# Kernel tuning notes

Measured on AMD Instinct MI355X. Metric: run time of the kernel, lower is better.

Reference implementation:

```python
import jax, jax.numpy as jnp
import numpy as np

jax.config.update("jax_enable_x64", True)  # needed for faithful float64 bit reinterpretation

VOCAB = 50257
HIDDEN = 1024
MAX_POS = 4096
TYPE_VOCAB = 2
NUM_FEATS = 94
PROJ_INTER = 256
NUM_TOKEN_ID = 5
LN_EPS = 1e-12


def _layer_norm(x, g, b, eps=LN_EPS):
    mu = jnp.mean(x, axis=-1, keepdims=True)
    var = jnp.var(x, axis=-1, keepdims=True)
    return (x - mu) * jax.lax.rsqrt(var + eps) * g + b


def _numeric_features(values, formats):
    # values: [B,S] float32 (torch casts to float64 internally), formats: [B,S] int
    v = values.astype(jnp.float64)
    # float64_binary_repr (64 bits). Torch: (int64_view & (1<<i)) > 0; bit 63 mask
    # overflows to INT64_MIN so (x & mask) > 0 is always False -> replicate exactly.
    bits = jax.lax.bitcast_convert_type(v, jnp.int64)
    masks = jnp.left_shift(jnp.int64(1), jnp.arange(64, dtype=jnp.int64))
    binary = ((bits[..., None] & masks) > 0).astype(jnp.float32)  # [B,S,64]
    av = jnp.abs(v)
    fl = jnp.floor(av)
    units = jnp.clip(fl % 10.0, 0, 9).astype(jnp.int32)
    oh_units = jax.nn.one_hot(units, 10, dtype=jnp.float32)       # [B,S,10]
    tens = jnp.clip((fl // 10.0) % 10.0, 0, 9).astype(jnp.int32)
    oh_tens = jax.nn.one_hot(tens, 10, dtype=jnp.float32)         # [B,S,10]
    log_v = jnp.log(av + 1e-6).astype(jnp.float32)
    sign = jnp.sign(v).astype(jnp.float32)
    expo = jnp.where(av > 1e-6, jnp.floor(jnp.log10(jnp.maximum(av, 1e-300))), 0.0).astype(jnp.float32)
    is_int = (av == fl).astype(jnp.float32)
    is_pos = (v > 0).astype(jnp.float32)
    is_zero = (v == 0.0).astype(jnp.float32)
    is_neg = (v < 0).astype(jnp.float32)
    pos_int = (v == jnp.floor(v)) & (v > 0)
    l2 = jnp.log2(jnp.maximum(v, 1.0))
    is_pow2 = (pos_int & (l2 == jnp.floor(l2))).astype(jnp.float32)
    fmt_int = (formats == 0).astype(jnp.float32)
    fmt_float = (formats == 1).astype(jnp.float32)
    scalars = jnp.stack([log_v, sign, expo, is_int, is_pos, is_zero, is_neg, is_pow2, fmt_int, fmt_float], axis=-1)
    return jnp.concatenate([binary, oh_units, oh_tens, scalars], axis=-1)  # [B,S,94]


def setup_inputs() -> dict:
    key = jax.random.key(0)
    ks = jax.random.split(key, 12)
    B, S = 8, 2048
    input_ids = jax.random.randint(ks[0], (B, S), 0, VOCAB, dtype=jnp.int64)
    numeric_values = jax.random.normal(ks[1], (B, S), dtype=jnp.float32) * 100.0
    numeric_formats = jax.random.randint(ks[2], (B, S), 0, 2, dtype=jnp.int64)
    s = 0.02
    W_word = (jax.random.normal(ks[3], (VOCAB, HIDDEN), dtype=jnp.float32) * s).at[0].set(0.0)  # padding_idx=0
    W_pos = jax.random.normal(ks[4], (MAX_POS, HIDDEN), dtype=jnp.float32) * s
    W_type = jax.random.normal(ks[5], (TYPE_VOCAB, HIDDEN), dtype=jnp.float32) * s
    ln_g = jnp.ones((HIDDEN,), jnp.float32)
    ln_b = jnp.zeros((HIDDEN,), jnp.float32)
    p_w1 = jax.random.normal(ks[6], (NUM_FEATS, PROJ_INTER), dtype=jnp.float32) * s
    p_b1 = jnp.zeros((PROJ_INTER,), jnp.float32)
    p_w2 = jax.random.normal(ks[7], (PROJ_INTER, HIDDEN), dtype=jnp.float32) * s
    p_b2 = jnp.zeros((HIDDEN,), jnp.float32)
    pln_g = jnp.ones((HIDDEN,), jnp.float32)
    pln_b = jnp.zeros((HIDDEN,), jnp.float32)
    return dict(input_ids=input_ids, numeric_values=numeric_values, numeric_formats=numeric_formats,
                W_word=W_word, W_pos=W_pos, W_type=W_type, ln_g=ln_g, ln_b=ln_b,
                p_w1=p_w1, p_b1=p_b1, p_w2=p_w2, p_b2=p_b2, pln_g=pln_g, pln_b=pln_b)


def reference(input_ids, numeric_values, numeric_formats, W_word, W_pos, W_type,
              ln_g, ln_b, p_w1, p_b1, p_w2, p_b2, pln_g, pln_b):
    B, S = input_ids.shape
    # text embeddings: word + position + token_type (token_type_ids default = 0)
    text = W_word[input_ids] + W_pos[jnp.arange(S)][None, :, :] + W_type[0][None, None, :]
    text = text.astype(jnp.float32)
    # active numeric positions: [NUM] token AND non-NaN value
    active = (input_ids == NUM_TOKEN_ID) & ~jnp.isnan(numeric_values)  # [B,S]
    safe_vals = jnp.where(active, numeric_values, 1.0)
    feats = _numeric_features(safe_vals, numeric_formats)  # [B,S,94] float32
    # numeric projection MLP: Linear -> GELU -> Linear -> LayerNorm
    h = jax.nn.gelu(feats @ p_w1 + p_b1, approximate=False)
    num_emb = _layer_norm(h @ p_w2 + p_b2, pln_g, pln_b)
    num_emb = jnp.where(active[..., None], num_emb, 0.0)  # scatter into zeros
    # fusion_type == 'add', then final LayerNorm (dropout p=0 -> identity)
    out = _layer_norm(text + num_emb, ln_g, ln_b)
    return out
```

## Files before the change

kernel.cpp:

```cpp
#include <hip/hip_runtime.h>
#include <math.h>

#define HIDDEN 1024
#define SEQ 2048
#define NF 94
#define PI 256
#define NUM_TOKEN 5

typedef float vfloat4 __attribute__((ext_vector_type(4)));

__device__ __forceinline__ float gelu_exact(float a) {
    return 0.5f * a * (1.0f + erff(a * 0.70710678118654752f));
}

__global__ __launch_bounds__(256)
void blackhole_emb_kernel(const int* __restrict__ ids,
                          const float* __restrict__ vals,
                          const int* __restrict__ fmts,
                          const float* __restrict__ Ww,
                          const float* __restrict__ Wp,
                          const float* __restrict__ Wt,
                          const float* __restrict__ lng,
                          const float* __restrict__ lnb,
                          const float* __restrict__ w1,
                          const float* __restrict__ b1,
                          const float* __restrict__ w2,
                          const float* __restrict__ b2,
                          const float* __restrict__ plng,
                          const float* __restrict__ plnb,
                          float* __restrict__ out,
                          int tokens)
{
    const int lane  = threadIdx.x & 63;
    const int wv    = threadIdx.x >> 6;
    const int token = blockIdx.x * 4 + wv;
    if (token >= tokens) return;
    const int s = token & (SEQ - 1);

    const int   id     = ids[token];
    const float vraw   = vals[token];
    const bool  active = (id == NUM_TOKEN) && !isnan(vraw);

    const float* wrow = Ww + (size_t)id * HIDDEN;
    const float* prow = Wp + (size_t)s  * HIDDEN;
    const int    col0 = lane * 4;

    float x[4][4];
    #pragma unroll
    for (int j = 0; j < 4; ++j) {
        const int off = j * 256 + col0;
        const float4 aw = *(const float4*)(wrow + off);
        const float4 ap = *(const float4*)(prow + off);
        const float4 at = *(const float4*)(Wt   + off);
        x[j][0] = aw.x + ap.x + at.x;
        x[j][1] = aw.y + ap.y + at.y;
        x[j][2] = aw.z + ap.z + at.z;
        x[j][3] = aw.w + ap.w + at.w;
    }

    if (active) {
        const double    v    = (double)vraw;
        const double    av   = fabs(v);
        const long long bits = __double_as_longlong(v);
        const double    fl   = floor(av);
        const int       fmt  = fmts[token];

        float f0 = (lane < 63 && ((bits >> lane) & 1LL)) ? 1.0f : 0.0f;
        float f1 = 0.0f;
        if (lane < 10) {
            const int units = (int)fmin(fmax(fmod(fl, 10.0), 0.0), 9.0);
            f1 = (lane == units) ? 1.0f : 0.0f;
        } else if (lane < 20) {
            const int tens = (int)fmin(fmax(fmod(floor(fl / 10.0), 10.0), 0.0), 9.0);
            f1 = (lane - 10 == tens) ? 1.0f : 0.0f;
        } else if (lane < 30) {
            switch (lane - 20) {
                case 0: f1 = (float)log(av + 1e-6); break;
                case 1: f1 = (v > 0.0) ? 1.0f : ((v < 0.0) ? -1.0f : 0.0f); break;
                case 2: f1 = (av > 1e-6) ? (float)floor(log10(fmax(av, 1e-300))) : 0.0f; break;
                case 3: f1 = (av == fl) ? 1.0f : 0.0f; break;
                case 4: f1 = (v > 0.0) ? 1.0f : 0.0f; break;
                case 5: f1 = (v == 0.0) ? 1.0f : 0.0f; break;
                case 6: f1 = (v < 0.0) ? 1.0f : 0.0f; break;
                case 7: {
                    const bool   pos_int = (v == floor(v)) && (v > 0.0);
                    const double l2      = log2(fmax(v, 1.0));
                    f1 = (pos_int && (l2 == floor(l2))) ? 1.0f : 0.0f;
                    break;
                }
                case 8: f1 = (fmt == 0) ? 1.0f : 0.0f; break;
                case 9: f1 = (fmt == 1) ? 1.0f : 0.0f; break;
            }
        }

        float acc[4] = { b1[lane], b1[lane + 64], b1[lane + 128], b1[lane + 192] };
        for (int k = 0; k < 64; ++k) {
            const float  fk  = __shfl(f0, k, 64);
            const float* col = w1 + k * PI;
            acc[0] = fmaf(fk, col[lane],       acc[0]);
            acc[1] = fmaf(fk, col[lane + 64],  acc[1]);
            acc[2] = fmaf(fk, col[lane + 128], acc[2]);
            acc[3] = fmaf(fk, col[lane + 192], acc[3]);
        }
        for (int k = 0; k < NF - 64; ++k) {
            const float  fk  = __shfl(f1, k, 64);
            const float* col = w1 + (64 + k) * PI;
            acc[0] = fmaf(fk, col[lane],       acc[0]);
            acc[1] = fmaf(fk, col[lane + 64],  acc[1]);
            acc[2] = fmaf(fk, col[lane + 128], acc[2]);
            acc[3] = fmaf(fk, col[lane + 192], acc[3]);
        }
        float h[4];
        #pragma unroll
        for (int i = 0; i < 4; ++i) h[i] = gelu_exact(acc[i]);

        float n[4][4];
        #pragma unroll
        for (int j = 0; j < 4; ++j) {
            const float4 bb = *(const float4*)(b2 + j * 256 + col0);
            n[j][0] = bb.x; n[j][1] = bb.y; n[j][2] = bb.z; n[j][3] = bb.w;
        }
        #pragma unroll
        for (int i = 0; i < 4; ++i) {
            for (int kk = 0; kk < 64; ++kk) {
                const float  hk  = __shfl(h[i], kk, 64);
                const float* row = w2 + (size_t)(i * 64 + kk) * HIDDEN;
                #pragma unroll
                for (int j = 0; j < 4; ++j) {
                    const float4 w = *(const float4*)(row + j * 256 + col0);
                    n[j][0] = fmaf(hk, w.x, n[j][0]);
                    n[j][1] = fmaf(hk, w.y, n[j][1]);
                    n[j][2] = fmaf(hk, w.z, n[j][2]);
                    n[j][3] = fmaf(hk, w.w, n[j][3]);
                }
            }
        }

        float sm = 0.0f, sq = 0.0f;
        #pragma unroll
        for (int j = 0; j < 4; ++j)
            #pragma unroll
            for (int c = 0; c < 4; ++c) { sm += n[j][c]; sq += n[j][c] * n[j][c]; }
        #pragma unroll
        for (int off = 32; off > 0; off >>= 1) {
            sm += __shfl_xor(sm, off, 64);
            sq += __shfl_xor(sq, off, 64);
        }
        const float mu   = sm * (1.0f / HIDDEN);
        const float var  = sq * (1.0f / HIDDEN) - mu * mu;
        const float rstd = rsqrtf(var + 1e-12f);
        #pragma unroll
        for (int j = 0; j < 4; ++j) {
            const float4 g4 = *(const float4*)(plng + j * 256 + col0);
            const float4 b4 = *(const float4*)(plnb + j * 256 + col0);
            x[j][0] += (n[j][0] - mu) * rstd * g4.x + b4.x;
            x[j][1] += (n[j][1] - mu) * rstd * g4.y + b4.y;
            x[j][2] += (n[j][2] - mu) * rstd * g4.z + b4.z;
            x[j][3] += (n[j][3] - mu) * rstd * g4.w + b4.w;
        }
    }

    float sm = 0.0f, sq = 0.0f;
    #pragma unroll
    for (int j = 0; j < 4; ++j)
        #pragma unroll
        for (int c = 0; c < 4; ++c) { sm += x[j][c]; sq += x[j][c] * x[j][c]; }
    #pragma unroll
    for (int off = 32; off > 0; off >>= 1) {
        sm += __shfl_xor(sm, off, 64);
        sq += __shfl_xor(sq, off, 64);
    }
    const float mu   = sm * (1.0f / HIDDEN);
    const float var  = sq * (1.0f / HIDDEN) - mu * mu;
    const float rstd = rsqrtf(var + 1e-12f);

    float* orow = out + (size_t)token * HIDDEN;
    #pragma unroll
    for (int j = 0; j < 4; ++j) {
        const int off = j * 256 + col0;
        const float4 g4 = *(const float4*)(lng + off);
        const float4 b4 = *(const float4*)(lnb + off);
        vfloat4 o;
        o.x = (x[j][0] - mu) * rstd * g4.x + b4.x;
        o.y = (x[j][1] - mu) * rstd * g4.y + b4.y;
        o.z = (x[j][2] - mu) * rstd * g4.z + b4.z;
        o.w = (x[j][3] - mu) * rstd * g4.w + b4.w;
        __builtin_nontemporal_store(o, (vfloat4*)(orow + off));
    }
}

extern "C" void kernel_launch(void* const* d_in, const int* in_sizes, int n_in,
                              void* d_out, int out_size, void* d_ws, size_t ws_size,
                              hipStream_t stream) {
    const int*   ids  = (const int*)d_in[0];
    const float* vals = (const float*)d_in[1];
    const int*   fmts = (const int*)d_in[2];
    const float* Ww   = (const float*)d_in[3];
    const float* Wp   = (const float*)d_in[4];
    const float* Wt   = (const float*)d_in[5];
    const float* lng  = (const float*)d_in[6];
    const float* lnb  = (const float*)d_in[7];
    const float* w1   = (const float*)d_in[8];
    const float* b1   = (const float*)d_in[9];
    const float* w2   = (const float*)d_in[10];
    const float* b2   = (const float*)d_in[11];
    const float* plng = (const float*)d_in[12];
    const float* plnb = (const float*)d_in[13];
    float* out = (float*)d_out;

    const int tokens = in_sizes[0];
    const int blocks = (tokens + 3) / 4;
    blackhole_emb_kernel<<<blocks, 256, 0, stream>>>(
        ids, vals, fmts, Ww, Wp, Wt, lng, lnb, w1, b1, w2, b2, plng, plnb, out, tokens);
}
```

Before: 305.3 us.

## Split embedding into text-LN kernel and sparse numeric fixup kernel

The fused kernel is split in two. One kernel computes embedding plus LayerNorm for every token using 512-thread blocks with a strided token mapping. A second small kernel uses ballot to find the active numeric tokens, recomputes them with the MLP path, and overwrites their output rows. This removes divergent MLP work from the main bandwidth-bound pass, at the cost of a second launch, rewritten rows, and a fixup kernel limited to 64 single-wave blocks that serialises the active tokens within each wave.

```diff
diff --git a/kernel.cpp b/kernel.cpp
--- a/kernel.cpp
+++ b/kernel.cpp
@@ -13,8 +13,71 @@
     return 0.5f * a * (1.0f + erff(a * 0.70710678118654752f));
 }
 
-__global__ __launch_bounds__(256)
-void blackhole_emb_kernel(const int* __restrict__ ids,
+__global__ __launch_bounds__(512, 8)
+void text_ln_kernel(const int* __restrict__ ids,
+                    const float* __restrict__ Ww,
+                    const float* __restrict__ Wp,
+                    const float* __restrict__ Wt,
+                    const float* __restrict__ lng,
+                    const float* __restrict__ lnb,
+                    float* __restrict__ out,
+                    int tokens)
+{
+    const int lane = threadIdx.x & 63;
+    const int wv   = threadIdx.x >> 6;
+    const int token = (int)blockIdx.x + wv * (int)gridDim.x;
+    if (token >= tokens) return;
+    const int s = token & (SEQ - 1);
+
+    const int id = ids[token];
+    const float* wrow = Ww + (size_t)id * HIDDEN;
+    const float* prow = Wp + (size_t)s  * HIDDEN;
+    const int    col0 = lane * 4;
+
+    float x[4][4];
+    #pragma unroll
+    for (int j = 0; j < 4; ++j) {
+        const int off = j * 256 + col0;
+        const float4 aw = *(const float4*)(wrow + off);
+        const float4 ap = *(const float4*)(prow + off);
+        const float4 at = *(const float4*)(Wt   + off);
+        x[j][0] = aw.x + ap.x + at.x;
+        x[j][1] = aw.y + ap.y + at.y;
+        x[j][2] = aw.z + ap.z + at.z;
+        x[j][3] = aw.w + ap.w + at.w;
+    }
+
+    float sm = 0.0f, sq = 0.0f;
+    #pragma unroll
+    for (int j = 0; j < 4; ++j)
+        #pragma unroll
+        for (int c = 0; c < 4; ++c) { sm += x[j][c]; sq += x[j][c] * x[j][c]; }
+    #pragma unroll
+    for (int off = 32; off > 0; off >>= 1) {
+        sm += __shfl_xor(sm, off, 64);
+        sq += __shfl_xor(sq, off, 64);
+    }
+    const float mu   = sm * (1.0f / HIDDEN);
+    const float var  = sq * (1.0f / HIDDEN) - mu * mu;
+    const float rstd = rsqrtf(var + 1e-12f);
+
+    float* orow = out + (size_t)token * HIDDEN;
+    #pragma unroll
+    for (int j = 0; j < 4; ++j) {
+        const int off = j * 256 + col0;
+        const float4 g4 = *(const float4*)(lng + off);
+        const float4 b4 = *(const float4*)(lnb + off);
+        vfloat4 o;
+        o.x = (x[j][0] - mu) * rstd * g4.x + b4.x;
+        o.y = (x[j][1] - mu) * rstd * g4.y + b4.y;
+        o.z = (x[j][2] - mu) * rstd * g4.z + b4.z;
+        o.w = (x[j][3] - mu) * rstd * g4.w + b4.w;
+        __builtin_nontemporal_store(o, (vfloat4*)(orow + off));
+    }
+}
+
+__global__ __launch_bounds__(64)
+void numeric_fixup_kernel(const int* __restrict__ ids,
                           const float* __restrict__ vals,
                           const int* __restrict__ fmts,
                           const float* __restrict__ Ww,
@@ -31,161 +94,170 @@
                           float* __restrict__ out,
                           int tokens)
 {
-    const int lane  = threadIdx.x & 63;
-    const int wv    = threadIdx.x >> 6;
-    const int token = blockIdx.x * 4 + wv;
-    if (token >= tokens) return;
-    const int s = token & (SEQ - 1);
-
-    const int   id     = ids[token];
-    const float vraw   = vals[token];
-    const bool  active = (id == NUM_TOKEN) && !isnan(vraw);
-
-    const float* wrow = Ww + (size_t)id * HIDDEN;
-    const float* prow = Wp + (size_t)s  * HIDDEN;
-    const int    col0 = lane * 4;
-
-    float x[4][4];
-    #pragma unroll
-    for (int j = 0; j < 4; ++j) {
-        const int off = j * 256 + col0;
-        const float4 aw = *(const float4*)(wrow + off);
-        const float4 ap = *(const float4*)(prow + off);
-        const float4 at = *(const float4*)(Wt   + off);
-        x[j][0] = aw.x + ap.x + at.x;
-        x[j][1] = aw.y + ap.y + at.y;
-        x[j][2] = aw.z + ap.z + at.z;
-        x[j][3] = aw.w + ap.w + at.w;
-    }
-
-    if (active) {
-        const double    v    = (double)vraw;
-        const double    av   = fabs(v);
-        const long long bits = __double_as_longlong(v);
-        const double    fl   = floor(av);
-        const int       fmt  = fmts[token];
-
-        float f0 = (lane < 63 && ((bits >> lane) & 1LL)) ? 1.0f : 0.0f;
-        float f1 = 0.0f;
-        if (lane < 10) {
-            const int units = (int)fmin(fmax(fmod(fl, 10.0), 0.0), 9.0);
-            f1 = (lane == units) ? 1.0f : 0.0f;
-        } else if (lane < 20) {
-            const int tens = (int)fmin(fmax(fmod(floor(fl / 10.0), 10.0), 0.0), 9.0);
-            f1 = (lane - 10 == tens) ? 1.0f : 0.0f;
-        } else if (lane < 30) {
-            switch (lane - 20) {
-                case 0: f1 = (float)log(av + 1e-6); break;
-                case 1: f1 = (v > 0.0) ? 1.0f : ((v < 0.0) ? -1.0f : 0.0f); break;
-                case 2: f1 = (av > 1e-6) ? (float)floor(log10(fmax(av, 1e-300))) : 0.0f; break;
-                case 3: f1 = (av == fl) ? 1.0f : 0.0f; break;
-                case 4: f1 = (v > 0.0) ? 1.0f : 0.0f; break;
-                case 5: f1 = (v == 0.0) ? 1.0f : 0.0f; break;
-                case 6: f1 = (v < 0.0) ? 1.0f : 0.0f; break;
-                case 7: {
-                    const bool   pos_int = (v == floor(v)) && (v > 0.0);
-                    const double l2      = log2(fmax(v, 1.0));
-                    f1 = (pos_int && (l2 == floor(l2))) ? 1.0f : 0.0f;
-                    break;
-                }
-                case 8: f1 = (fmt == 0) ? 1.0f : 0.0f; break;
-                case 9: f1 = (fmt == 1) ? 1.0f : 0.0f; break;
-            }
+    const int lane = threadIdx.x & 63;
+
+    for (int base = (int)blockIdx.x * 64; base < tokens; base += (int)gridDim.x * 64) {
+        const int t = base + lane;
+        bool act = false;
+        if (t < tokens) {
+            const float vv = vals[t];
+            act = (ids[t] == NUM_TOKEN) && !isnan(vv);
         }
-
-        float acc[4] = { b1[lane], b1[lane + 64], b1[lane + 128], b1[lane + 192] };
-        for (int k = 0; k < 64; ++k) {
-            const float  fk  = __shfl(f0, k, 64);
-            const float* col = w1 + k * PI;
-            acc[0] = fmaf(fk, col[lane],       acc[0]);
-            acc[1] = fmaf(fk, col[lane + 64],  acc[1]);
-            acc[2] = fmaf(fk, col[lane + 128], acc[2]);
-            acc[3] = fmaf(fk, col[lane + 192], acc[3]);
+        unsigned long long m = __ballot(act);
+        while (m) {
+            const int bit = __ffsll(m) - 1;
+            m &= (m - 1ULL);
+            const int token = base + bit;
+            const int s     = token & (SEQ - 1);
+            const float vraw = vals[token];
+            const int   fmt  = fmts[token];
+
+            const float* wrow = Ww + (size_t)NUM_TOKEN * HIDDEN;
+            const float* prow = Wp + (size_t)s * HIDDEN;
+            const int    col0 = lane * 4;
+
+            float x[4][4];
+            #pragma unroll
+            for (int j = 0; j < 4; ++j) {
+                const int off = j * 256 + col0;
+                const float4 aw = *(const float4*)(wrow + off);
+                const float4 ap = *(const float4*)(prow + off);
+                const float4 at = *(const float4*)(Wt   + off);
+                x[j][0] = aw.x + ap.x + at.x;
+                x[j][1] = aw.y + ap.y + at.y;
+                x[j][2] = aw.z + ap.z + at.z;
+                x[j][3] = aw.w + ap.w + at.w;
+            }
+
+            const double    v    = (double)vraw;
+            const double    av   = fabs(v);
+            const long long bits = __double_as_longlong(v);
+            const double    fl   = floor(av);
+
+            float f0 = (lane < 63 && ((bits >> lane) & 1LL)) ? 1.0f : 0.0f;
+            float f1 = 0.0f;
+            if (lane < 10) {
+                const int units = (int)fmin(fmax(fmod(fl, 10.0), 0.0), 9.0);
+                f1 = (lane == units) ? 1.0f : 0.0f;
+            } else if (lane < 20) {
+                const int tens = (int)fmin(fmax(fmod(floor(fl / 10.0), 10.0), 0.0), 9.0);
+                f1 = (lane - 10 == tens) ? 1.0f : 0.0f;
+            } else if (lane < 30) {
+                switch (lane - 20) {
+                    case 0: f1 = (float)log(av + 1e-6); break;
+                    case 1: f1 = (v > 0.0) ? 1.0f : ((v < 0.0) ? -1.0f : 0.0f); break;
+                    case 2: f1 = (av > 1e-6) ? (float)floor(log10(fmax(av, 1e-300))) : 0.0f; break;
+                    case 3: f1 = (av == fl) ? 1.0f : 0.0f; break;
+                    case 4: f1 = (v > 0.0) ? 1.0f : 0.0f; break;
+                    case 5: f1 = (v == 0.0) ? 1.0f : 0.0f; break;
+                    case 6: f1 = (v < 0.0) ? 1.0f : 0.0f; break;
+                    case 7: {
+                        const bool   pos_int = (v == floor(v)) && (v > 0.0);
+                        const double l2      = log2(fmax(v, 1.0));
+                        f1 = (pos_int && (l2 == floor(l2))) ? 1.0f : 0.0f;
+                        break;
+                    }
+                    case 8: f1 = (fmt == 0) ? 1.0f : 0.0f; break;
+                    case 9: f1 = (fmt == 1) ? 1.0f : 0.0f; break;
+                }
+            }
+
+            float acc[4] = { b1[lane], b1[lane + 64], b1[lane + 128], b1[lane + 192] };
+            for (int k = 0; k < 64; ++k) {
+                const float  fk  = __shfl(f0, k, 64);
+                const float* col = w1 + k * PI;
+                acc[0] = fmaf(fk, col[lane],       acc[0]);
+                acc[1] = fmaf(fk, col[lane + 64],  acc[1]);
+                acc[2] = fmaf(fk, col[lane + 128], acc[2]);
+                acc[3] = fmaf(fk, col[lane + 192], acc[3]);
+            }
+            for (int k = 0; k < NF - 64; ++k) {
+                const float  fk  = __shfl(f1, k, 64);
+                const float* col = w1 + (64 + k) * PI;
+                acc[0] = fmaf(fk, col[lane],       acc[0]);
+                acc[1] = fmaf(fk, col[lane + 64],  acc[1]);
+                acc[2] = fmaf(fk, col[lane + 128], acc[2]);
+                acc[3] = fmaf(fk, col[lane + 192], acc[3]);
+            }
+            float h[4];
+            #pragma unroll
+            for (int i = 0; i < 4; ++i) h[i] = gelu_exact(acc[i]);
+
+            float n[4][4];
+            #pragma unroll
+            for (int j = 0; j < 4; ++j) {
+                const float4 bb = *(const float4*)(b2 + j * 256 + col0);
+                n[j][0] = bb.x; n[j][1] = bb.y; n[j][2] = bb.z; n[j][3] = bb.w;
+            }
+            #pragma unroll
+            for (int i = 0; i < 4; ++i) {
+                for (int kk = 0; kk < 64; ++kk) {
+                    const float  hk  = __shfl(h[i], kk, 64);
+                    const float* row = w2 + (size_t)(i * 64 + kk) * HIDDEN;
+                    #pragma unroll
+                    for (int j = 0; j < 4; ++j) {
+                        const float4 w = *(const float4*)(row + j * 256 + col0);
+                        n[j][0] = fmaf(hk, w.x, n[j][0]);
+                        n[j][1] = fmaf(hk, w.y, n[j][1]);
+                        n[j][2] = fmaf(hk, w.z, n[j][2]);
+                        n[j][3] = fmaf(hk, w.w, n[j][3]);
+                    }
+                }
+            }
+
+            {
+                float sm = 0.0f, sq = 0.0f;
+                #pragma unroll
+                for (int j = 0; j < 4; ++j)
+                    #pragma unroll
+                    for (int c = 0; c < 4; ++c) { sm += n[j][c]; sq += n[j][c] * n[j][c]; }
+                #pragma unroll
+                for (int off = 32; off > 0; off >>= 1) {
+                    sm += __shfl_xor(sm, off, 64);
+                    sq += __shfl_xor(sq, off, 64);
+                }
+                const float mu   = sm * (1.0f / HIDDEN);
+                const float var  = sq * (1.0f / HIDDEN) - mu * mu;
+                const float rstd = rsqrtf(var + 1e-12f);
+                #pragma unroll
+                for (int j = 0; j < 4; ++j) {
+                    const float4 g4 = *(const float4*)(plng + j * 256 + col0);
+                    const float4 b4 = *(const float4*)(plnb + j * 256 + col0);
+                    x[j][0] += (n[j][0] - mu) * rstd * g4.x + b4.x;
+                    x[j][1] += (n[j][1] - mu) * rstd * g4.y + b4.y;
+                    x[j][2] += (n[j][2] - mu) * rstd * g4.z + b4.z;
+                    x[j][3] += (n[j][3] - mu) * rstd * g4.w + b4.w;
+                }
+            }
+
+            float sm = 0.0f, sq = 0.0f;
+            #pragma unroll
+            for (int j = 0; j < 4; ++j)
+                #pragma unroll
+                for (int c = 0; c < 4; ++c) { sm += x[j][c]; sq += x[j][c] * x[j][c]; }
+            #pragma unroll
+            for (int off = 32; off > 0; off >>= 1) {
+                sm += __shfl_xor(sm, off, 64);
+                sq += __shfl_xor(sq, off, 64);
+            }
+            const float mu   = sm * (1.0f / HIDDEN);
+            const float var  = sq * (1.0f / HIDDEN) - mu * mu;
+            const float rstd = rsqrtf(var + 1e-12f);
+
+            float* orow = out + (size_t)token * HIDDEN;
+            #pragma unroll
+            for (int j = 0; j < 4; ++j) {
+                const int off = j * 256 + col0;
+                const float4 g4 = *(const float4*)(lng + off);
+                const float4 b4 = *(const float4*)(lnb + off);
+                float4 o;
+                o.x = (x[j][0] - mu) * rstd * g4.x + b4.x;
+                o.y = (x[j][1] - mu) * rstd * g4.y + b4.y;
+                o.z = (x[j][2] - mu) * rstd * g4.z + b4.z;
+                o.w = (x[j][3] - mu) * rstd * g4.w + b4.w;
+                *(float4*)(orow + off) = o;
+            }
         }
-        for (int k = 0; k < NF - 64; ++k) {
-            const float  fk  = __shfl(f1, k, 64);
-            const float* col = w1 + (64 + k) * PI;
-            acc[0] = fmaf(fk, col[lane],       acc[0]);
-            acc[1] = fmaf(fk, col[lane + 64],  acc[1]);
-            acc[2] = fmaf(fk, col[lane + 128], acc[2]);
-            acc[3] = fmaf(fk, col[lane + 192], acc[3]);
-        }
-        float h[4];
-        #pragma unroll
-        for (int i = 0; i < 4; ++i) h[i] = gelu_exact(acc[i]);
-
-        float n[4][4];
-        #pragma unroll
-        for (int j = 0; j < 4; ++j) {
-            const float4 bb = *(const float4*)(b2 + j * 256 + col0);
-            n[j][0] = bb.x; n[j][1] = bb.y; n[j][2] = bb.z; n[j][3] = bb.w;
-        }
-        #pragma unroll
-        for (int i = 0; i < 4; ++i) {
-            for (int kk = 0; kk < 64; ++kk) {
-                const float  hk  = __shfl(h[i], kk, 64);
-                const float* row = w2 + (size_t)(i * 64 + kk) * HIDDEN;
-                #pragma unroll
-                for (int j = 0; j < 4; ++j) {
-                    const float4 w = *(const float4*)(row + j * 256 + col0);
-                    n[j][0] = fmaf(hk, w.x, n[j][0]);
-                    n[j][1] = fmaf(hk, w.y, n[j][1]);
-                    n[j][2] = fmaf(hk, w.z, n[j][2]);
-                    n[j][3] = fmaf(hk, w.w, n[j][3]);
-                }
-            }
-        }
-
-        float sm = 0.0f, sq = 0.0f;
-        #pragma unroll
-        for (int j = 0; j < 4; ++j)
-            #pragma unroll
-            for (int c = 0; c < 4; ++c) { sm += n[j][c]; sq += n[j][c] * n[j][c]; }
-        #pragma unroll
-        for (int off = 32; off > 0; off >>= 1) {
-            sm += __shfl_xor(sm, off, 64);
-            sq += __shfl_xor(sq, off, 64);
-        }
-        const float mu   = sm * (1.0f / HIDDEN);
-        const float var  = sq * (1.0f / HIDDEN) - mu * mu;
-        const float rstd = rsqrtf(var + 1e-12f);
-        #pragma unroll
-        for (int j = 0; j < 4; ++j) {
-            const float4 g4 = *(const float4*)(plng + j * 256 + col0);
-            const float4 b4 = *(const float4*)(plnb + j * 256 + col0);
-            x[j][0] += (n[j][0] - mu) * rstd * g4.x + b4.x;
-            x[j][1] += (n[j][1] - mu) * rstd * g4.y + b4.y;
-            x[j][2] += (n[j][2] - mu) * rstd * g4.z + b4.z;
-            x[j][3] += (n[j][3] - mu) * rstd * g4.w + b4.w;
-        }
-    }
-
-    float sm = 0.0f, sq = 0.0f;
-    #pragma unroll
-    for (int j = 0; j < 4; ++j)
-        #pragma unroll
-        for (int c = 0; c < 4; ++c) { sm += x[j][c]; sq += x[j][c] * x[j][c]; }
-    #pragma unroll
-    for (int off = 32; off > 0; off >>= 1) {
-        sm += __shfl_xor(sm, off, 64);
-        sq += __shfl_xor(sq, off, 64);
-    }
-    const float mu   = sm * (1.0f / HIDDEN);
-    const float var  = sq * (1.0f / HIDDEN) - mu * mu;
-    const float rstd = rsqrtf(var + 1e-12f);
-
-    float* orow = out + (size_t)token * HIDDEN;
-    #pragma unroll
-    for (int j = 0; j < 4; ++j) {
-        const int off = j * 256 + col0;
-        const float4 g4 = *(const float4*)(lng + off);
-        const float4 b4 = *(const float4*)(lnb + off);
-        vfloat4 o;
-        o.x = (x[j][0] - mu) * rstd * g4.x + b4.x;
-        o.y = (x[j][1] - mu) * rstd * g4.y + b4.y;
-        o.z = (x[j][2] - mu) * rstd * g4.z + b4.z;
-        o.w = (x[j][3] - mu) * rstd * g4.w + b4.w;
-        __builtin_nontemporal_store(o, (vfloat4*)(orow + off));
     }
 }
 
@@ -208,8 +280,10 @@
     const float* plnb = (const float*)d_in[13];
     float* out = (float*)d_out;
 
-    const int tokens = in_sizes[0];
-    const int blocks = (tokens + 3) / 4;
-    blackhole_emb_kernel<<<blocks, 256, 0, stream>>>(
+    const int tokens  = in_sizes[0];
+    const int blocksA = (tokens + 7) / 8;
+    text_ln_kernel<<<blocksA, 512, 0, stream>>>(
+        ids, Ww, Wp, Wt, lng, lnb, out, tokens);
+    numeric_fixup_kernel<<<64, 64, 0, stream>>>(
         ids, vals, fmts, Ww, Wp, Wt, lng, lnb, w1, b1, w2, b2, plng, plnb, out, tokens);
 }
```

Result: slower. 320.3 us (+4.9%).
